# Kernel optimization log

Measured on AMD Instinct MI355X. Metric: run time of the kernel, lower is better.

Reference implementation:

```python
import jax, jax.numpy as jnp
import numpy as np
from jax.scipy.special import gammaln

T, NGRID, NMUL, LENF = 365, 2000, 8, 15
PRECS = 1e-5
DT = 1.0
# parameter bounds in the order of self.parameters_bound
BOUNDS = np.array([
    [0.0, 1.0],    # pctim
    [1.0, 2000.0], # smax
    [0.005, 0.995],# f1
    [0.005, 0.995],# f2
    [0.0, 1.0],    # kuz
    [0.0, 7.0],    # rexp
    [0.005, 0.995],# f3
    [0.005, 0.995],# f4
    [0.0, 1.0],    # pfree
    [0.0, 1.0],    # klzp
    [0.0, 1.0],    # klzs
], dtype=np.float32)
ROUT_BOUNDS = np.array([[0.0, 2.9], [0.0, 6.5]], dtype=np.float32)


def setup_inputs() -> dict:
    key = jax.random.key(0)
    k1, k2, k3, k4 = jax.random.split(key, 4)
    x = jax.random.uniform(k1, (T, NGRID, 4), dtype=jnp.float32)
    # scale forcings to realistic ranges: prcp [0,15] mm/d, tmax/tmin C, pet [0,6] mm/d
    x = x * jnp.array([15.0, 30.0, 15.0, 6.0], dtype=jnp.float32)
    c = jax.random.uniform(k2, (NGRID, 2), dtype=jnp.float32)
    params_raw = jax.random.uniform(k3, (T, NGRID, 11, NMUL), dtype=jnp.float32)
    conv_params_hydro = jax.random.uniform(k4, (NGRID, 2), dtype=jnp.float32)
    return {"x_hydro_model": x, "c_hydro_model": c,
            "params_raw": params_raw, "conv_params_hydro": conv_params_hydro}


def _soilmoisture_1(S1, S1max, S2, S2max):
    mask = (S1 / S1max < S2 / S2max).astype(S1.dtype)
    return (S2 * S1max - S1 * S2max) / (S1max + S2max) * mask


def _soilmoisture_2(S1, S1max, S2, S2max, S3, S3max):
    part1 = S2 * (S1 * (S2max + S3max) + S1max * (S2 + S3)) / (
        (S2max + S3max) * (S1max + S2max + S3max))
    mask = (S1 / S1max < (S2 + S3) / (S2max + S3max)).astype(S1.dtype)
    return part1 * mask


def _evap_7(S, Smax, Ep, dt):
    return jnp.minimum(S / Smax * Ep, S / dt)


def _evap_1(S, Ep, dt):
    return jnp.minimum(S / dt, Ep)


def _saturation_1(In, S, Smax):
    return In * (S >= Smax).astype(In.dtype)


def _percolation_4(p1, p2, p3, p4, p5, S, Smax, dt):
    S_rel = jnp.maximum(1e-8, S / Smax)
    demand = p1 * (1.0 + p2 * (p4 / p5) ** (1.0 + p3))
    return jnp.maximum(1e-8, jnp.minimum(S / dt, S_rel * demand))


def _deficit_based_distribution(S1, S1max, S2, S2max):
    rd1 = (S1max - S1) / S1max
    rd2 = (S2max - S2) / S2max
    total_rd = rd1 + rd2
    mask = (total_rd != 0.0).astype(S1.dtype)
    safe = jnp.where(total_rd != 0.0, total_rd, 1.0)
    total_max = S1max + S2max
    return rd1 / safe * mask + S1max / total_max * (1.0 - mask)


def _uh_gamma(a, b, lenF):
    # a, b: [lenF, Ngrid]
    aa = jax.nn.relu(a) + 0.1
    theta = jax.nn.relu(b) + 0.5
    t = (jnp.arange(lenF, dtype=a.dtype) + 0.5)[:, None]  # [lenF, 1]
    w = jnp.exp(-gammaln(aa)) * theta ** (-aa) * t ** (aa - 1.0) * jnp.exp(-t / theta)
    return w / w.sum(0)


def _uh_conv(q, w):
    # q: [T, Ngrid], w: [lenF, Ngrid]; causal convolution y[t]=sum_k w[k]*q[t-k]
    conv1 = lambda xi, wi: jnp.convolve(xi, wi)[:q.shape[0]]
    return jax.vmap(conv1, in_axes=(1, 1), out_axes=1)(q, w)


def _step(carry, inp):
    uztw, uzfw, lztw, lzfwp, lzfws = carry
    P, Ep, par = inp  # P, Ep: [Ngrid, nmul]; par: [11, Ngrid, nmul]
    pctim, smax, f1, f2, kuz, rexp, f3, f4, pfree, klzp, klzs = [par[i] for i in range(11)]

    uztwm = jnp.maximum(PRECS, f1 * smax)
    uzfwm = jnp.maximum(PRECS, f2 * (smax - uztwm))
    lztwm = jnp.maximum(PRECS, f3 * (smax - uztwm - uzfwm))
    lzfwpm = jnp.maximum(PRECS, f4 * (smax - uztwm - uzfwm - lztwm))
    lzfwsm = jnp.maximum(PRECS, (1.0 - f4) * (smax - uztwm - uzfwm - lztwm))
    pbase = lzfwpm * klzp + lzfwsm * klzs
    zperc = (lztwm + lzfwsm * (1.0 - klzs)) / pbase + lzfwpm * (1.0 - klzp) / pbase

    qdir = pctim * P                       # split_1: impervious direct runoff
    peff = (1.0 - pctim) * P
    ru = _soilmoisture_1(uztw, uztwm, uzfw, uzfwm)
    euztw = _evap_7(uztw, uztwm, Ep, DT)
    twexu = _saturation_1(peff, uztw, uztwm)
    qsur = _saturation_1(twexu, uzfw, uzfwm)
    qint = kuz * uzfw                      # interflow_5
    euzfw = _evap_1(uzfw, jax.nn.relu(Ep - euztw), DT)
    deficit = (jax.nn.relu(lztwm - lztw) + jax.nn.relu(lzfwpm - lzfwp)
               + jax.nn.relu(lzfwsm - lzfws))
    pc = _percolation_4(pbase, zperc, rexp, deficit,
                        lztwm + lzfwpm + lzfwsm, uzfw, uzfwm, DT)
    pctw = (1.0 - pfree) * pc
    pcfw = pfree * pc
    flz = _deficit_based_distribution(lzfwp, lzfwpm, lzfws, lzfwsm)
    pcfwp = flz * pcfw
    pcfws = (1.0 - flz) * pcfw
    rlp = _soilmoisture_2(lztw, lztwm, lzfwp, lzfwpm, lzfws, lzfwsm)
    rls = _soilmoisture_2(lztw, lztwm, lzfws, lzfwsm, lzfwp, lzfwpm)
    elztw = _evap_7(lztw, lztwm, jax.nn.relu(Ep - euztw - euzfw), DT)
    twexl = _saturation_1(pctw, lztw, lztwm)
    twexlp = flz * twexl
    twexls = (1.0 - flz) * twexl
    qbfp = klzp * lzfwp                    # baseflow_1
    qbfs = klzs * lzfws

    uztw_n = jnp.clip(uztw + peff + ru - euztw - twexu, PRECS, uztwm)
    uzfw_n = jnp.clip(uzfw + twexu - ru - euzfw - qint - qsur - pc, PRECS, uzfwm)
    lztw_n = jnp.clip(lztw + pctw - twexl + rlp + rls - elztw, PRECS, lztwm)
    lzfwp_n = jnp.clip(lzfwp + pcfwp + twexlp - rlp - qbfp, PRECS, lzfwpm)
    lzfws_n = jnp.clip(lzfws + pcfws + twexls - rls - qbfs, PRECS, lzfwsm)

    q = qdir + qsur + qint + qbfp + qbfs   # total runoff [mm/d]
    return (uztw_n, uzfw_n, lztw_n, lzfwp_n, lzfws_n), q


def _forward(x_hydro_model, c_hydro_model, params_raw, conv_params_hydro):
    nmul = params_raw.shape[-1]
    # scale raw params to physical bounds: [T, 11, Ngrid, nmul]
    b = jnp.asarray(BOUNDS)
    pars = jnp.transpose(params_raw, (0, 2, 1, 3))  # [T, 11, Ngrid, nmul]
    pars = pars * (b[:, 1] - b[:, 0])[None, :, None, None] + b[:, 0][None, :, None, None]

    Pm = jnp.broadcast_to(x_hydro_model[:, :, 0:1], (T, NGRID, nmul))
    PET = jnp.broadcast_to(x_hydro_model[:, :, 3:4], (T, NGRID, nmul))

    init = tuple(jnp.full((NGRID, nmul), 1e-4, dtype=jnp.float32) for _ in range(5))
    _, qsim = jax.lax.scan(_step, init, (Pm, PET, pars))  # qsim: [T, Ngrid, nmul]
    qmean = qsim.mean(-1)  # average over ensemble multiplier -> [T, Ngrid]

    # gamma unit-hydrograph routing
    routa = conv_params_hydro[:, 0] * (ROUT_BOUNDS[0, 1] - ROUT_BOUNDS[0, 0]) + ROUT_BOUNDS[0, 0]
    routb = conv_params_hydro[:, 1] * (ROUT_BOUNDS[1, 1] - ROUT_BOUNDS[1, 0]) + ROUT_BOUNDS[1, 0]
    a = jnp.broadcast_to(routa[None, :], (LENF, NGRID))
    bb = jnp.broadcast_to(routb[None, :], (LENF, NGRID))
    w = _uh_gamma(a, bb, LENF)             # [lenF, Ngrid]
    return _uh_conv(qmean, w)              # [T, Ngrid]


def reference(x_hydro_model, c_hydro_model, params_raw, conv_params_hydro):
    return _forward(x_hydro_model, c_hydro_model, params_raw, conv_params_hydro)
```

## Files before the change

### kernel.cpp

```cpp
#include <hip/hip_runtime.h>
#include <math.h>

namespace {

constexpr int kT = 365;
constexpr int kG = 2000;
constexpr int kM = 8;
constexpr int kF = 15;
constexpr float kPrecs = 1e-5f;

constexpr int kQBase = kF * kG;
constexpr int kWBase = (kF + kT) * kG;

__device__ __forceinline__ float rcpf(float v) { return __builtin_amdgcn_rcpf(v); }

template <int CTRL>
__device__ __forceinline__ float dpp_xadd(float v) {
    int r = __builtin_amdgcn_update_dpp(0, __float_as_int(v), CTRL, 0xF, 0xF, true);
    return v + __int_as_float(r);
}

struct Derived {
    float pctim, kuz, pfree, klzp, klzs;
    float uztwm, uzfwm, lztwm, lzfwpm, lzfwsm;
    float r_uztwm, r_uzfwm, r_lztwm, r_lzfwpm, r_lzfwsm, r_uzsum;
    float pbase, zperc, rexp1;
    float r_totalm, s23m, r_s23m, r_den, flz_fb;
};

__device__ __forceinline__ Derived make_derived(const float pr[11]) {
#pragma clang fp contract(fast)
    Derived d;
    d.pctim = pr[0];
    const float smax = pr[1] * 1999.f + 1.f;
    const float f1   = pr[2] * 0.99f + 0.005f;
    const float f2   = pr[3] * 0.99f + 0.005f;
    d.kuz            = pr[4];
    const float rexp = pr[5] * 7.f;
    const float f3   = pr[6] * 0.99f + 0.005f;
    const float f4   = pr[7] * 0.99f + 0.005f;
    d.pfree = pr[8]; d.klzp = pr[9]; d.klzs = pr[10];

    d.uztwm  = fmaxf(kPrecs, f1 * smax);
    d.uzfwm  = fmaxf(kPrecs, f2 * (smax - d.uztwm));
    d.lztwm  = fmaxf(kPrecs, f3 * (smax - d.uztwm - d.uzfwm));
    const float rem = smax - d.uztwm - d.uzfwm - d.lztwm;
    d.lzfwpm = fmaxf(kPrecs, f4 * rem);
    d.lzfwsm = fmaxf(kPrecs, (1.f - f4) * rem);

    d.pbase = d.lzfwpm * d.klzp + d.lzfwsm * d.klzs;
    const float r_pbase = rcpf(d.pbase);
    d.zperc = (d.lztwm + d.lzfwsm * (1.f - d.klzs)) * r_pbase
            + d.lzfwpm * (1.f - d.klzp) * r_pbase;
    d.rexp1 = 1.f + rexp;

    d.r_uztwm  = rcpf(d.uztwm);
    d.r_uzfwm  = rcpf(d.uzfwm);
    d.r_lztwm  = rcpf(d.lztwm);
    d.r_lzfwpm = rcpf(d.lzfwpm);
    d.r_lzfwsm = rcpf(d.lzfwsm);
    d.r_uzsum  = rcpf(d.uztwm + d.uzfwm);

    const float totalm = d.lztwm + d.lzfwpm + d.lzfwsm;
    d.s23m     = d.lzfwpm + d.lzfwsm;
    d.r_totalm = rcpf(totalm);
    d.r_s23m   = rcpf(d.s23m);
    d.r_den    = rcpf(d.s23m * totalm);
    d.flz_fb   = d.lzfwpm * d.r_s23m;
    return d;
}

struct PBuf { float pr[11]; float P, Ep; };

__global__ __launch_bounds__(64, 1) void sacsma_scan(
    const float* __restrict__ x,
    const float* __restrict__ params_raw,
    float* __restrict__ qs)
{
#pragma clang fp contract(fast)
    const int tid = blockIdx.x * 64 + threadIdx.x;
    const int g = tid >> 3;
    const int m = tid & 7;

    const size_t PS = (size_t)kG * 11 * kM;
    const size_t XS = (size_t)kG * 4;
    const float* pp = params_raw + (size_t)g * 11 * kM + m;
    const float* xp = x + (size_t)g * 4;

    float uztw = 1e-4f, uzfw = 1e-4f, lztw = 1e-4f, lzfwp = 1e-4f, lzfws = 1e-4f;

    PBuf A, B;

#define ISSUE(BUF, T3) do {                                          \
        const size_t _po = (size_t)(T3) * PS;                        \
        const size_t _xo = (size_t)(T3) * XS;                        \
        _Pragma("unroll")                                            \
        for (int _i = 0; _i < 11; ++_i) BUF.pr[_i] = pp[_po + _i * kM]; \
        BUF.P = xp[_xo]; BUF.Ep = xp[_xo + 3];                       \
    } while (0)

    ISSUE(A, 0);
    Derived d = make_derived(A.pr);
    float P = A.P, Ep = A.Ep;
    ISSUE(A, 1);
    ISSUE(B, 2);

    float q0 = 0.f, q1 = 0.f, q2 = 0.f, q3 = 0.f;

#define BODY(T, BUF, QREG) do {                                               \
                              \
        const float qdir = d.pctim * P;                                       \
        const float peff = (1.f - d.pctim) * P;                               \
        const float ratio_u1 = uztw * d.r_uztwm;                              \
        const float ratio_u2 = uzfw * d.r_uzfwm;                              \
        const float ru = (ratio_u1 < ratio_u2)                                \
            ? (uzfw * d.uztwm - uztw * d.uzfwm) * d.r_uzsum : 0.f;            \
        const float euztw = fminf(ratio_u1 * Ep, uztw);                       \
        const float twexu = (uztw >= d.uztwm) ? peff : 0.f;                   \
        const float qsur  = (uzfw >= d.uzfwm) ? twexu : 0.f;                  \
        const float qint  = d.kuz * uzfw;                                     \
        const float euzfw = fminf(uzfw, fmaxf(Ep - euztw, 0.f));              \
        const float deficit = fmaxf(d.lztwm - lztw, 0.f)                      \
            + fmaxf(d.lzfwpm - lzfwp, 0.f) + fmaxf(d.lzfwsm - lzfws, 0.f);    \
        const float xrel = deficit * d.r_totalm;                              \
        const float powv = exp2f(d.rexp1 * __log2f(xrel));                    \
        const float demand = d.pbase * (1.f + d.zperc * powv);                \
        const float srel = fmaxf(1e-8f, ratio_u2);                            \
        const float pc   = fmaxf(1e-8f, fminf(uzfw, srel * demand));          \
        const float pctw = (1.f - d.pfree) * pc;                              \
        const float pcfw = d.pfree * pc;                                      \
        const float rd1 = (d.lzfwpm - lzfwp) * d.r_lzfwpm;                    \
        const float rd2 = (d.lzfwsm - lzfws) * d.r_lzfwsm;                    \
        const float trd = rd1 + rd2;                                          \
        const float flz = (trd != 0.f) ? rd1 * rcpf(trd) : d.flz_fb;          \
        const float pcfwp = flz * pcfw;                                       \
        const float pcfws = (1.f - flz) * pcfw;                               \
        const float lsum = lzfwp + lzfws;                                     \
        const float ratio_l = lztw * d.r_lztwm;                               \
        const bool  lmask = ratio_l < lsum * d.r_s23m;                        \
        const float nume = (lztw * d.s23m + d.lztwm * lsum) * d.r_den;        \
        const float rlp = lmask ? lzfwp * nume : 0.f;                         \
        const float rls = lmask ? lzfws * nume : 0.f;                         \
        const float elztw = fminf(ratio_l * fmaxf(Ep - euztw - euzfw, 0.f), lztw); \
        const float twexl = (lztw >= d.lztwm) ? pctw : 0.f;                   \
        const float twexlp = flz * twexl;                                     \
        const float twexls = (1.f - flz) * twexl;                             \
        const float qbfp = d.klzp * lzfwp;                                    \
        const float qbfs = d.klzs * lzfws;                                    \
        uztw  = fminf(fmaxf(uztw + peff + ru - euztw - twexu, kPrecs), d.uztwm);   \
        uzfw  = fminf(fmaxf(uzfw + twexu - ru - euzfw - qint - qsur - pc, kPrecs), d.uzfwm); \
        lztw  = fminf(fmaxf(lztw + pctw - twexl + rlp + rls - elztw, kPrecs), d.lztwm);      \
        lzfwp = fminf(fmaxf(lzfwp + pcfwp + twexlp - rlp - qbfp, kPrecs), d.lzfwpm);         \
        lzfws = fminf(fmaxf(lzfws + pcfws + twexls - rls - qbfs, kPrecs), d.lzfwsm);         \
        QREG = qdir + qsur + qint + qbfp + qbfs;                              \
         \
        const float _Pn = BUF.P, _En = BUF.Ep;                                \
        const Derived _dn = make_derived(BUF.pr);                             \
        if ((T) + 3 < kT) ISSUE(BUF, (T) + 3);                                \
        d = _dn; P = _Pn; Ep = _En;                                           \
    } while (0)

#define FLUSH(TB) do {                                                        \
        q0 = dpp_xadd<0xB1>(q0); q1 = dpp_xadd<0xB1>(q1);                     \
        q2 = dpp_xadd<0xB1>(q2); q3 = dpp_xadd<0xB1>(q3);                     \
        q0 = dpp_xadd<0x4E>(q0); q1 = dpp_xadd<0x4E>(q1);                     \
        q2 = dpp_xadd<0x4E>(q2); q3 = dpp_xadd<0x4E>(q3);                     \
        q0 += __shfl_xor(q0, 4); q1 += __shfl_xor(q1, 4);                     \
        q2 += __shfl_xor(q2, 4); q3 += __shfl_xor(q3, 4);                     \
        const float _v01 = (m & 1) ? q1 : q0;                                 \
        const float _v23 = (m & 1) ? q3 : q2;                                 \
        const float _v = (m & 2) ? _v23 : _v01;                               \
        if (m < 4) qs[(size_t)((TB) + m) * kG + g] = _v;                      \
    } while (0)

    for (int t = 0; t < 357; t += 4) {
        BODY(t,     A, q0);
        BODY(t + 1, B, q1);
        BODY(t + 2, A, q2);
        BODY(t + 3, B, q3);
        FLUSH(t);
    }
    BODY(360, A, q0);
    BODY(361, B, q1);
    BODY(362, A, q2);
    BODY(363, B, q3);
    FLUSH(360);
    BODY(364, A, q0);
    q0 = dpp_xadd<0xB1>(q0);
    q0 = dpp_xadd<0x4E>(q0);
    q0 += __shfl_xor(q0, 4);
    if (m == 0) qs[(size_t)364 * kG + g] = q0;

#undef BODY
#undef ISSUE
#undef FLUSH
}

__global__ void uh_weights(const float* __restrict__ conv_params,
                           float* __restrict__ wbuf)
{
    const int g = blockIdx.x * blockDim.x + threadIdx.x;
    if (g >= kG) return;
    const float aa = fmaxf(conv_params[2 * g] * 2.9f, 0.f) + 0.1f;
    const float th = fmaxf(conv_params[2 * g + 1] * 6.5f, 0.f) + 0.5f;
    const float cw = expf(-lgammaf(aa)) * powf(th, -aa);
    float w[kF];
    float s = 0.f;
#pragma unroll
    for (int k = 0; k < kF; ++k) {
        const float tt = (float)k + 0.5f;
        w[k] = cw * powf(tt, aa - 1.f) * expf(-tt / th);
        s += w[k];
    }
    const float inv = 0.125f / s;
#pragma unroll
    for (int k = 0; k < kF; ++k) wbuf[k * kG + g] = w[k] * inv;
}

__global__ void uh_conv(const float* __restrict__ ws,
                        float* __restrict__ out)
{
    const int tid = blockIdx.x * blockDim.x + threadIdx.x;
    if (tid >= kT * kG) return;
    const int t = tid / kG;
    const int g = tid - t * kG;
    const float* q = ws + kQBase;
    const float* w = ws + kWBase;
    float y = 0.f;
#pragma unroll
    for (int k = 0; k < kF; ++k)
        y += w[k * kG + g] * q[(ptrdiff_t)(t - k) * kG + g];
    out[(size_t)t * kG + g] = y;
}

}

extern "C" void kernel_launch(void* const* d_in, const int* in_sizes, int n_in,
                              void* d_out, int out_size, void* d_ws, size_t ws_size,
                              hipStream_t stream) {
    const float* x           = (const float*)d_in[0];
    const float* params_raw  = (const float*)d_in[2];
    const float* conv_params = (const float*)d_in[3];
    float* out = (float*)d_out;
    float* ws  = (float*)d_ws;

    (void)hipMemsetAsync(ws, 0, (size_t)kF * kG * sizeof(float), stream);

    uh_weights<<<(kG + 255) / 256, 256, 0, stream>>>(conv_params, ws + kWBase);
    sacsma_scan<<<(kG * kM) / 64, 64, 0, stream>>>(x, params_raw, ws + kQBase);
    uh_conv<<<(kT * kG + 255) / 256, 256, 0, stream>>>(ws, out);
}
```

Before: 178.0 us.

## Simplify per-step algebra, pointer-bump prefetch, split ensemble reduction into conv

Rewrites several per-step expressions to drop reciprocals. The demand term becomes pbase + Zp*pow, flz is computed from cross-multiplied deficits, and the lower-zone mask compares by cross-multiplication, which shrinks the Derived struct and the per-step rcp work. Prefetch addressing now bumps pointers instead of recomputing offsets from the time index. When workspace allows, the scan stores two half-ensemble partial sums per timestep and skips the cross-lane shuffle. The conv kernel then adds the two halves, trading an extra load per tap and a larger workspace for a shorter serial scan step.

New measurement: 202.0 us. 13.5% more time.

```diff
diff --git a/kernel.cpp b/kernel.cpp
--- a/kernel.cpp
+++ b/kernel.cpp
@@ -9,8 +9,14 @@
 constexpr int kF = 15;
 constexpr float kPrecs = 1e-5f;
 
-constexpr int kQBase = kF * kG;
-constexpr int kWBase = (kF + kT) * kG;
+constexpr int kPadH  = kF * 2 * kG;
+constexpr int kQH    = kPadH;
+constexpr int kWH    = kPadH + kT * 2 * kG;
+constexpr size_t kNeedH = (size_t)(kWH + kF * kG) * 4;
+
+constexpr int kPadF  = kF * kG;
+constexpr int kQF    = kPadF;
+constexpr int kWF    = kPadF + kT * kG;
 
 __device__ __forceinline__ float rcpf(float v) { return __builtin_amdgcn_rcpf(v); }
 
@@ -23,9 +29,9 @@
 struct Derived {
     float pctim, kuz, pfree, klzp, klzs;
     float uztwm, uzfwm, lztwm, lzfwpm, lzfwsm;
-    float r_uztwm, r_uzfwm, r_lztwm, r_lzfwpm, r_lzfwsm, r_uzsum;
-    float pbase, zperc, rexp1;
-    float r_totalm, s23m, r_s23m, r_den, flz_fb;
+    float r_uztwm, r_uzfwm, r_lztwm, r_uzsum;
+    float pbase, Zp, rexp1;
+    float r_totalm, s23m, r_den, flz_fb;
 };
 
 __device__ __forceinline__ Derived make_derived(const float pr[11]) {
@@ -48,30 +54,26 @@
     d.lzfwpm = fmaxf(kPrecs, f4 * rem);
     d.lzfwsm = fmaxf(kPrecs, (1.f - f4) * rem);
 
-    d.pbase = d.lzfwpm * d.klzp + d.lzfwsm * d.klzs;
-    const float r_pbase = rcpf(d.pbase);
-    d.zperc = (d.lztwm + d.lzfwsm * (1.f - d.klzs)) * r_pbase
-            + d.lzfwpm * (1.f - d.klzp) * r_pbase;
-    d.rexp1 = 1.f + rexp;
+    const float totalm = d.lztwm + d.lzfwpm + d.lzfwsm;
+    d.pbase  = d.lzfwpm * d.klzp + d.lzfwsm * d.klzs;
+    d.Zp     = totalm - d.pbase;
+    d.rexp1  = 1.f + rexp;
 
     d.r_uztwm  = rcpf(d.uztwm);
     d.r_uzfwm  = rcpf(d.uzfwm);
     d.r_lztwm  = rcpf(d.lztwm);
-    d.r_lzfwpm = rcpf(d.lzfwpm);
-    d.r_lzfwsm = rcpf(d.lzfwsm);
     d.r_uzsum  = rcpf(d.uztwm + d.uzfwm);
 
-    const float totalm = d.lztwm + d.lzfwpm + d.lzfwsm;
     d.s23m     = d.lzfwpm + d.lzfwsm;
     d.r_totalm = rcpf(totalm);
-    d.r_s23m   = rcpf(d.s23m);
     d.r_den    = rcpf(d.s23m * totalm);
-    d.flz_fb   = d.lzfwpm * d.r_s23m;
+    d.flz_fb   = d.lzfwpm * rcpf(d.s23m);
     return d;
 }
 
 struct PBuf { float pr[11]; float P, Ep; };
 
+template <bool HALF>
 __global__ __launch_bounds__(64, 1) void sacsma_scan(
     const float* __restrict__ x,
     const float* __restrict__ params_raw,
@@ -82,33 +84,41 @@
     const int g = tid >> 3;
     const int m = tid & 7;
 
-    const size_t PS = (size_t)kG * 11 * kM;
-    const size_t XS = (size_t)kG * 4;
-    const float* pp = params_raw + (size_t)g * 11 * kM + m;
-    const float* xp = x + (size_t)g * 4;
+    constexpr size_t PS = (size_t)kG * 11 * kM;
+    constexpr size_t XS = (size_t)kG * 4;
 
     float uztw = 1e-4f, uzfw = 1e-4f, lztw = 1e-4f, lzfwp = 1e-4f, lzfws = 1e-4f;
 
+    const float* p0 = params_raw + (size_t)g * 88 + m;
+    const float* x0 = x + (size_t)g * 4;
+    float pr0[11];
+#pragma unroll
+    for (int i = 0; i < 11; ++i) pr0[i] = p0[i * 8];
+    Derived d = make_derived(pr0);
+    float P = x0[0], Ep = x0[3];
+
+    const float* pA = p0 + PS;
+    const float* pB = p0 + 2 * PS;
+    const float* xA = x0 + XS;
+    const float* xB = x0 + 2 * XS;
+
     PBuf A, B;
-
-#define ISSUE(BUF, T3) do {                                          \
-        const size_t _po = (size_t)(T3) * PS;                        \
-        const size_t _xo = (size_t)(T3) * XS;                        \
-        _Pragma("unroll")                                            \
-        for (int _i = 0; _i < 11; ++_i) BUF.pr[_i] = pp[_po + _i * kM]; \
-        BUF.P = xp[_xo]; BUF.Ep = xp[_xo + 3];                       \
-    } while (0)
-
-    ISSUE(A, 0);
-    Derived d = make_derived(A.pr);
-    float P = A.P, Ep = A.Ep;
-    ISSUE(A, 1);
-    ISSUE(B, 2);
+#pragma unroll
+    for (int i = 0; i < 11; ++i) A.pr[i] = pA[i * 8];
+    A.P = xA[0]; A.Ep = xA[3];
+    pA += 2 * PS; xA += 2 * XS;
+#pragma unroll
+    for (int i = 0; i < 11; ++i) B.pr[i] = pB[i * 8];
+    B.P = xB[0]; B.Ep = xB[3];
+    pB += 2 * PS; xB += 2 * XS;
+
+    float* qp;
+    if (HALF) qp = qs + ((size_t)((m & 3) * 2 + (m >> 2))) * kG + g;
+    else      qp = qs + (size_t)m * kG + g;
 
     float q0 = 0.f, q1 = 0.f, q2 = 0.f, q3 = 0.f;
 
-#define BODY(T, BUF, QREG) do {                                               \
-                              \
+#define FLUX(QREG) do {                                                       \
         const float qdir = d.pctim * P;                                       \
         const float peff = (1.f - d.pctim) * P;                               \
         const float ratio_u1 = uztw * d.r_uztwm;                              \
@@ -124,20 +134,20 @@
             + fmaxf(d.lzfwpm - lzfwp, 0.f) + fmaxf(d.lzfwsm - lzfws, 0.f);    \
         const float xrel = deficit * d.r_totalm;                              \
         const float powv = exp2f(d.rexp1 * __log2f(xrel));                    \
-        const float demand = d.pbase * (1.f + d.zperc * powv);                \
+        const float demand = d.pbase + d.Zp * powv;                           \
         const float srel = fmaxf(1e-8f, ratio_u2);                            \
         const float pc   = fmaxf(1e-8f, fminf(uzfw, srel * demand));          \
         const float pctw = (1.f - d.pfree) * pc;                              \
         const float pcfw = d.pfree * pc;                                      \
-        const float rd1 = (d.lzfwpm - lzfwp) * d.r_lzfwpm;                    \
-        const float rd2 = (d.lzfwsm - lzfws) * d.r_lzfwsm;                    \
-        const float trd = rd1 + rd2;                                          \
-        const float flz = (trd != 0.f) ? rd1 * rcpf(trd) : d.flz_fb;          \
+        const float n1 = (d.lzfwpm - lzfwp) * d.lzfwsm;                       \
+        const float n2 = (d.lzfwsm - lzfws) * d.lzfwpm;                       \
+        const float ns = n1 + n2;                                             \
+        const float flz = (ns != 0.f) ? n1 * rcpf(ns) : d.flz_fb;             \
         const float pcfwp = flz * pcfw;                                       \
         const float pcfws = (1.f - flz) * pcfw;                               \
         const float lsum = lzfwp + lzfws;                                     \
         const float ratio_l = lztw * d.r_lztwm;                               \
-        const bool  lmask = ratio_l < lsum * d.r_s23m;                        \
+        const bool  lmask = lztw * d.s23m < lsum * d.lztwm;                   \
         const float nume = (lztw * d.s23m + d.lztwm * lsum) * d.r_den;        \
         const float rlp = lmask ? lzfwp * nume : 0.f;                         \
         const float rls = lmask ? lzfws * nume : 0.f;                         \
@@ -147,52 +157,79 @@
         const float twexls = (1.f - flz) * twexl;                             \
         const float qbfp = d.klzp * lzfwp;                                    \
         const float qbfs = d.klzs * lzfws;                                    \
+        QREG = qdir + qsur + qint + qbfp + qbfs;                              \
         uztw  = fminf(fmaxf(uztw + peff + ru - euztw - twexu, kPrecs), d.uztwm);   \
         uzfw  = fminf(fmaxf(uzfw + twexu - ru - euzfw - qint - qsur - pc, kPrecs), d.uzfwm); \
         lztw  = fminf(fmaxf(lztw + pctw - twexl + rlp + rls - elztw, kPrecs), d.lztwm);      \
         lzfwp = fminf(fmaxf(lzfwp + pcfwp + twexlp - rlp - qbfp, kPrecs), d.lzfwpm);         \
         lzfws = fminf(fmaxf(lzfws + pcfws + twexls - rls - qbfs, kPrecs), d.lzfwsm);         \
-        QREG = qdir + qsur + qint + qbfp + qbfs;                              \
-         \
+    } while (0)
+
+#define BODY(BUF, PP, XP, QREG) do {                                          \
+        FLUX(QREG);                                                           \
         const float _Pn = BUF.P, _En = BUF.Ep;                                \
         const Derived _dn = make_derived(BUF.pr);                             \
-        if ((T) + 3 < kT) ISSUE(BUF, (T) + 3);                                \
+        _Pragma("unroll")                                                     \
+        for (int _i = 0; _i < 11; ++_i) BUF.pr[_i] = PP[_i * 8];              \
+        BUF.P = XP[0]; BUF.Ep = XP[3];                                        \
+        PP += 2 * PS; XP += 2 * XS;                                           \
         d = _dn; P = _Pn; Ep = _En;                                           \
     } while (0)
 
-#define FLUSH(TB) do {                                                        \
+#define BODY_NI(BUF, QREG) do {                                               \
+        FLUX(QREG);                                                           \
+        const float _Pn = BUF.P, _En = BUF.Ep;                                \
+        const Derived _dn = make_derived(BUF.pr);                             \
+        d = _dn; P = _Pn; Ep = _En;                                           \
+    } while (0)
+
+#define FLUSH() do {                                                          \
         q0 = dpp_xadd<0xB1>(q0); q1 = dpp_xadd<0xB1>(q1);                     \
         q2 = dpp_xadd<0xB1>(q2); q3 = dpp_xadd<0xB1>(q3);                     \
         q0 = dpp_xadd<0x4E>(q0); q1 = dpp_xadd<0x4E>(q1);                     \
         q2 = dpp_xadd<0x4E>(q2); q3 = dpp_xadd<0x4E>(q3);                     \
-        q0 += __shfl_xor(q0, 4); q1 += __shfl_xor(q1, 4);                     \
-        q2 += __shfl_xor(q2, 4); q3 += __shfl_xor(q3, 4);                     \
-        const float _v01 = (m & 1) ? q1 : q0;                                 \
-        const float _v23 = (m & 1) ? q3 : q2;                                 \
-        const float _v = (m & 2) ? _v23 : _v01;                               \
-        if (m < 4) qs[(size_t)((TB) + m) * kG + g] = _v;                      \
+        if (HALF) {                                                           \
+            const float _v01 = (m & 1) ? q1 : q0;                             \
+            const float _v23 = (m & 1) ? q3 : q2;                             \
+            const float _v = (m & 2) ? _v23 : _v01;                           \
+            qp[0] = _v;                                \
+            qp += 8 * kG;                                                     \
+        } else {                                                              \
+            q0 += __shfl_xor(q0, 4); q1 += __shfl_xor(q1, 4);                 \
+            q2 += __shfl_xor(q2, 4); q3 += __shfl_xor(q3, 4);                 \
+            const float _v01 = (m & 1) ? q1 : q0;                             \
+            const float _v23 = (m & 1) ? q3 : q2;                             \
+            const float _v = (m & 2) ? _v23 : _v01;                           \
+            if (m < 4) qp[0] = _v;                                            \
+            qp += 4 * kG;                                                     \
+        }                                                                     \
     } while (0)
 
     for (int t = 0; t < 357; t += 4) {
-        BODY(t,     A, q0);
-        BODY(t + 1, B, q1);
-        BODY(t + 2, A, q2);
-        BODY(t + 3, B, q3);
-        FLUSH(t);
-    }
-    BODY(360, A, q0);
-    BODY(361, B, q1);
-    BODY(362, A, q2);
-    BODY(363, B, q3);
-    FLUSH(360);
-    BODY(364, A, q0);
+        BODY(A, pA, xA, q0);
+        BODY(B, pB, xB, q1);
+        BODY(A, pA, xA, q2);
+        BODY(B, pB, xB, q3);
+        FLUSH();
+    }
+    BODY(A, pA, xA, q0);
+    BODY(B, pB, xB, q1);
+    BODY_NI(A, q2);
+    BODY_NI(B, q3);
+    FLUSH();
+    FLUX(q0);
     q0 = dpp_xadd<0xB1>(q0);
     q0 = dpp_xadd<0x4E>(q0);
-    q0 += __shfl_xor(q0, 4);
-    if (m == 0) qs[(size_t)364 * kG + g] = q0;
-
+    if (HALF) {
+        if ((m & 3) == 0) qp[0] = q0;
+    } else {
+        q0 += __shfl_xor(q0, 4);
+        if (m == 0) qp[0] = q0;
+    }
+
+#undef FLUX
 #undef BODY
-#undef ISSUE
+#undef BODY_NI
 #undef FLUSH
 }
 
@@ -217,19 +254,24 @@
     for (int k = 0; k < kF; ++k) wbuf[k * kG + g] = w[k] * inv;
 }
 
-__global__ void uh_conv(const float* __restrict__ ws,
+template <bool HALF>
+__global__ void uh_conv(const float* __restrict__ qbase,
+                        const float* __restrict__ wbase,
                         float* __restrict__ out)
 {
     const int tid = blockIdx.x * blockDim.x + threadIdx.x;
     if (tid >= kT * kG) return;
     const int t = tid / kG;
     const int g = tid - t * kG;
-    const float* q = ws + kQBase;
-    const float* w = ws + kWBase;
     float y = 0.f;
 #pragma unroll
-    for (int k = 0; k < kF; ++k)
-        y += w[k * kG + g] * q[(ptrdiff_t)(t - k) * kG + g];
+    for (int k = 0; k < kF; ++k) {
+        const ptrdiff_t tk = (ptrdiff_t)(t - k);
+        float qv;
+        if (HALF) qv = qbase[tk * 2 * kG + g] + qbase[tk * 2 * kG + kG + g];
+        else      qv = qbase[tk * kG + g];
+        y += wbase[k * kG + g] * qv;
+    }
     out[(size_t)t * kG + g] = y;
 }
 
@@ -244,9 +286,16 @@
     float* out = (float*)d_out;
     float* ws  = (float*)d_ws;
 
-    (void)hipMemsetAsync(ws, 0, (size_t)kF * kG * sizeof(float), stream);
-
-    uh_weights<<<(kG + 255) / 256, 256, 0, stream>>>(conv_params, ws + kWBase);
-    sacsma_scan<<<(kG * kM) / 64, 64, 0, stream>>>(x, params_raw, ws + kQBase);
-    uh_conv<<<(kT * kG + 255) / 256, 256, 0, stream>>>(ws, out);
-}
+    const int nconv = (kT * kG + 255) / 256;
+    if (ws_size >= kNeedH) {
+        (void)hipMemsetAsync(ws, 0, (size_t)kPadH * sizeof(float), stream);
+        uh_weights<<<(kG + 255) / 256, 256, 0, stream>>>(conv_params, ws + kWH);
+        sacsma_scan<true><<<(kG * kM) / 64, 64, 0, stream>>>(x, params_raw, ws + kQH);
+        uh_conv<true><<<nconv, 256, 0, stream>>>(ws + kQH, ws + kWH, out);
+    } else {
+        (void)hipMemsetAsync(ws, 0, (size_t)kPadF * sizeof(float), stream);
+        uh_weights<<<(kG + 255) / 256, 256, 0, stream>>>(conv_params, ws + kWF);
+        sacsma_scan<false><<<(kG * kM) / 64, 64, 0, stream>>>(x, params_raw, ws + kQF);
+        uh_conv<false><<<nconv, 256, 0, stream>>>(ws + kQF, ws + kWF, out);
+    }
+}
```
